# Performance work log

Measured on AMD Instinct MI355X. Metric: run time of the kernel, lower is better.

The kernel has to match this reference:

```python
import jax, jax.numpy as jnp
import numpy as np

B, H_, W_, C, HEADS, WS, SR = 4, 56, 56, 256, 8, 3, 4
HD = C // HEADS
N = H_ * W_
LL = WS * WS
PH, PW = H_ // SR, W_ // SR
PL = PH * PW
K_TAB = 2048


def _unfold3(x, H, W):
    # x: (B, C, H, W) -> (B, C, 9, H*W); matches torch nn.Unfold(kernel_size=3, padding=1)
    xp = jnp.pad(x, ((0, 0), (0, 0), (1, 1), (1, 1)))
    pats = jnp.stack([xp[:, :, i:i + H, j:j + W] for i in range(3) for j in range(3)], axis=2)
    return pats.reshape(x.shape[0], x.shape[1], 9, H * W)


def _l2n(x):
    # torch F.normalize(dim=-1) with eps=1e-12
    return x / jnp.maximum(jnp.linalg.norm(x, axis=-1, keepdims=True), 1e-12)


def setup_inputs() -> dict:
    key = jax.random.key(0)
    ks = jax.random.split(key, 24)
    x = jax.random.normal(ks[0], (B, N, C), jnp.float32)
    # padding mask from unfold of ones image (True where window element falls outside)
    ones = np.zeros((H_ + 2, W_ + 2), np.float32)
    ones[1:-1, 1:-1] = 1.0
    pats = np.stack([ones[i:i + H_, j:j + W_] for i in range(3) for j in range(3)], 0).reshape(9, N)
    padding_mask = jnp.asarray((pats == 0).T)  # (N, 9) bool
    local_valid = LL - padding_mask.sum(-1)
    seq_length_scale = jnp.log(local_valid.astype(jnp.float32) + PL)[:, None]  # (N,1)
    relative_pos_index = jax.random.randint(ks[1], (N * PL,), 0, K_TAB)
    relative_coords_table = jax.random.uniform(ks[2], (K_TAB, 2), jnp.float32, -1.0, 1.0)
    w = lambda k, shape: jax.random.normal(k, shape, jnp.float32) * 0.02
    inp = dict(
        x=x, H=H_, W=W_,
        relative_pos_index=relative_pos_index,
        relative_coords_table=relative_coords_table,
        seq_length_scale=seq_length_scale,
        padding_mask=padding_mask,
        q_w=w(ks[3], (C, C)), q_b=jnp.zeros((C,), jnp.float32),
        kv_w=w(ks[4], (2 * C, C)), kv_b=jnp.zeros((2 * C,), jnp.float32),
        sr_w=w(ks[5], (C, C)), sr_b=jnp.zeros((C,), jnp.float32),
        norm_g=jnp.ones((C,), jnp.float32), norm_b=jnp.zeros((C,), jnp.float32),
        cpb1_w=w(ks[6], (512, 2)), cpb1_b=jnp.zeros((512,), jnp.float32),
        cpb2_w=w(ks[7], (HEADS, 512)), cpb2_b=jnp.zeros((HEADS,), jnp.float32),
        temperature=jnp.log(jnp.exp(jnp.ones((HEADS, 1, 1), jnp.float32) / 0.24) - 1.0),
        query_embedding=w(ks[8], (HEADS, 1, HD)),
        rel_pos_bias_local=jax.random.normal(ks[9], (HEADS, LL), jnp.float32) * 0.0004,
        learnable_tokens=w(ks[10], (HEADS, HD, LL)),
        learnable_bias=jnp.zeros((HEADS, 1, LL), jnp.float32),
        proj_w=w(ks[11], (C, C)), proj_b=jnp.zeros((C,), jnp.float32),
    )
    return inp


def reference(x, H, W, relative_pos_index, relative_coords_table, seq_length_scale,
              padding_mask, q_w, q_b, kv_w, kv_b, sr_w, sr_b, norm_g, norm_b,
              cpb1_w, cpb1_b, cpb2_w, cpb2_b, temperature, query_embedding,
              rel_pos_bias_local, learnable_tokens, learnable_bias, proj_w, proj_b):
    Bsz, n, Cd = x.shape
    h, hd, ll = HEADS, HD, LL
    pH, pW = H // SR, W // SR
    pL = pH * pW
    # ----- queries -----
    q = (x @ q_w.T + q_b).reshape(Bsz, n, h, hd).transpose(0, 2, 1, 3)  # (B,h,N,d)
    q_norm = _l2n(q)
    q_scaled = (q_norm + query_embedding) * jax.nn.softplus(temperature) * seq_length_scale
    # ----- local branch: unfolded window KV -----
    kv = x @ kv_w.T + kv_b  # (B,N,2C)
    k_loc, v_loc = jnp.split(kv, 2, axis=-1)
    k_loc = _l2n(k_loc.reshape(Bsz, n, h, hd)).reshape(Bsz, n, Cd)
    kv_img = jnp.concatenate([k_loc, v_loc], -1).transpose(0, 2, 1).reshape(Bsz, 2 * Cd, H, W)
    pats = _unfold3(kv_img, H, W).reshape(Bsz, 2 * h, hd, ll, n).transpose(0, 1, 4, 2, 3)  # (B,2h,N,d,ll)
    k_local, v_local = jnp.split(pats, 2, axis=1)
    attn_local = jnp.einsum('bhnd,bhndl->bhnl', q_scaled, k_local) + rel_pos_bias_local[:, None, :]
    attn_local = jnp.where(padding_mask, -jnp.inf, attn_local)
    # ----- global branch: 1x1 conv -> GELU -> avg pool -> LN -> KV -----
    x_img = x.transpose(0, 2, 1).reshape(Bsz, Cd, H, W)
    x_sr = jax.nn.gelu(jnp.einsum('oc,bchw->bohw', sr_w, x_img) + sr_b[None, :, None, None], approximate=False)
    x_pool = x_sr.reshape(Bsz, Cd, pH, SR, pW, SR).mean(axis=(3, 5)).reshape(Bsz, Cd, pL).transpose(0, 2, 1)
    mu = x_pool.mean(-1, keepdims=True)
    var = x_pool.var(-1, keepdims=True)
    x_pool = (x_pool - mu) / jnp.sqrt(var + 1e-5) * norm_g + norm_b
    kvp = (x_pool @ kv_w.T + kv_b).reshape(Bsz, pL, 2 * h, hd).transpose(0, 2, 1, 3)
    k_pool, v_pool = jnp.split(kvp, 2, axis=1)  # each (B,h,pL,d)
    # CPB-MLP relative position bias (interpolate is identity since test==trained resolution)
    tab = jax.nn.relu(relative_coords_table @ cpb1_w.T + cpb1_b) @ cpb2_w.T + cpb2_b  # (K,h)
    pool_bias = tab.T[:, relative_pos_index].reshape(h, n, pL)
    attn_pool = jnp.einsum('bhnd,bhmd->bhnm', q_scaled, _l2n(k_pool)) + pool_bias
    # ----- joint softmax over [local | pool] -----
    attn = jax.nn.softmax(jnp.concatenate([attn_local, attn_pool], axis=-1), axis=-1)
    a_loc, a_pool = attn[..., :ll], attn[..., ll:]
    w_loc = jnp.einsum('bhnd,hdl->bhnl', q_norm, learnable_tokens) + learnable_bias + a_loc
    x_local = jnp.einsum('bhnl,bhndl->bhnd', w_loc, v_local)
    x_glob = jnp.einsum('bhnm,bhmd->bhnd', a_pool, v_pool)
    out = (x_local + x_glob).transpose(0, 2, 1, 3).reshape(Bsz, n, Cd)
    return out @ proj_w.T + proj_b
```

## Files before the change

### kernel.cpp

```cpp
#include <hip/hip_runtime.h>
#include <hip/hip_bf16.h>
#include <math.h>

#define Bn   4
#define Hh   56
#define Wn   56
#define Cn   256
#define NHn  8
#define HDn  32
#define Nn   3136
#define LLn  9
#define PLn  196
#define PWn  14
#define KTABn 2048
#define Mrows 12544
#define MP   224

#define XCNT   3211264
#define QWOFF  XCNT
#define KVWOFF (QWOFF + 65536)
#define SRWOFF (KVWOFF + 131072)
#define PWOFF  (SRWOFF + 65536)
#define TOTCVT (PWOFF + 65536)

typedef __attribute__((ext_vector_type(8))) short short8v;
typedef __attribute__((ext_vector_type(4))) float float4v;

__device__ __forceinline__ unsigned short f2b(float f) {
  __hip_bfloat16 h = __float2bfloat16(f);
  return *(unsigned short*)&h;
}
__device__ __forceinline__ float b2f(unsigned short u) {
  union { unsigned int i; float f; } x; x.i = ((unsigned int)u) << 16; return x.f;
}
__device__ __forceinline__ void u4_to8f(uint4 u, float* o) {
  o[0]=b2f((unsigned short)(u.x&0xffff)); o[1]=b2f((unsigned short)(u.x>>16));
  o[2]=b2f((unsigned short)(u.y&0xffff)); o[3]=b2f((unsigned short)(u.y>>16));
  o[4]=b2f((unsigned short)(u.z&0xffff)); o[5]=b2f((unsigned short)(u.z>>16));
  o[6]=b2f((unsigned short)(u.w&0xffff)); o[7]=b2f((unsigned short)(u.w>>16));
}

__launch_bounds__(256)
__global__ void cvt5(const float* __restrict__ x, const float* __restrict__ qw,
                     const float* __restrict__ kvw, const float* __restrict__ srw,
                     const float* __restrict__ pw, unsigned short* __restrict__ dst)
{
  const int i = (blockIdx.x * 256 + threadIdx.x) * 4;
  const float* src; int off;
  if      (i < XCNT)   { src = x;   off = 0; }
  else if (i < KVWOFF) { src = qw;  off = QWOFF; }
  else if (i < SRWOFF) { src = kvw; off = KVWOFF; }
  else if (i < PWOFF)  { src = srw; off = SRWOFF; }
  else                 { src = pw;  off = PWOFF; }
  const float4 v = *(const float4*)(src + (i - off));
  ushort4 o2;
  o2.x = f2b(v.x); o2.y = f2b(v.y); o2.z = f2b(v.z); o2.w = f2b(v.w);
  *(ushort4*)(dst + i) = o2;
}

template <int MODE>
__launch_bounds__(512)
__global__ void mgemm(const unsigned short* __restrict__ A,
                      const unsigned short* __restrict__ Wb,
                      const float* __restrict__ b0, const float* __restrict__ b1,
                      const float* __restrict__ b2, void* __restrict__ Cv, int Nc,
                      const float* __restrict__ sls, const float* __restrict__ qe,
                      const float* __restrict__ temp, float* __restrict__ Mq)
{
  __shared__ __align__(16) unsigned char smem[34816];
  unsigned short* As = (unsigned short*)smem;
  unsigned short* Bs = (unsigned short*)(smem + 16384);
  const int t = threadIdx.x;
  const int w = t >> 6, lane = t & 63;
  const int q = lane >> 4, ln = lane & 15;
  const int n0 = blockIdx.x * 128, m0 = blockIdx.y * 128;
  const int wm = (w >> 1) * 32, wn = (w & 1) * 64;

  float4v acc[2][4];
  #pragma unroll
  for (int mt = 0; mt < 2; ++mt)
    #pragma unroll
    for (int nt = 0; nt < 4; ++nt)
      acc[mt][nt] = (float4v){0.f, 0.f, 0.f, 0.f};

  for (int k0 = 0; k0 < 256; k0 += 64) {
    #pragma unroll
    for (int j = 0; j < 2; ++j) {
      const int u = t + 512 * j;
      const int r = u >> 3, cg = u & 7;
      const int cs = cg ^ (r & 7);
      const uint4 av = *(const uint4*)(A  + (size_t)(m0 + r) * 256 + k0 + cg * 8);
      *(uint4*)(As + r * 64 + cs * 8) = av;
      const uint4 bv = *(const uint4*)(Wb + (size_t)(n0 + r) * 256 + k0 + cg * 8);
      *(uint4*)(Bs + r * 64 + cs * 8) = bv;
    }
    __syncthreads();
    #pragma unroll
    for (int kk = 0; kk < 2; ++kk) {
      short8v af[2], bfr[4];
      const int cg = kk * 4 + q;
      #pragma unroll
      for (int mt = 0; mt < 2; ++mt) {
        const int r = wm + mt * 16 + ln;
        af[mt] = *(const short8v*)(As + r * 64 + (cg ^ (r & 7)) * 8);
      }
      #pragma unroll
      for (int nt = 0; nt < 4; ++nt) {
        const int r = wn + nt * 16 + ln;
        bfr[nt] = *(const short8v*)(Bs + r * 64 + (cg ^ (r & 7)) * 8);
      }
      #pragma unroll
      for (int mt = 0; mt < 2; ++mt)
        #pragma unroll
        for (int nt = 0; nt < 4; ++nt)
          acc[mt][nt] = __builtin_amdgcn_mfma_f32_16x16x32_bf16(af[mt], bfr[nt], acc[mt][nt], 0, 0, 0);
    }
    __syncthreads();
  }

  if constexpr (MODE == 0) {
    float* C = (float*)Cv;
    float* tileF = (float*)smem;
    float bia[4];
    #pragma unroll
    for (int nt = 0; nt < 4; ++nt) bia[nt] = b0[n0 + wn + nt * 16 + ln];
    #pragma unroll
    for (int half = 0; half < 2; ++half) {
      if ((w >> 2) == half) {
        #pragma unroll
        for (int mt = 0; mt < 2; ++mt)
          #pragma unroll
          for (int r = 0; r < 4; ++r)
            #pragma unroll
            for (int nt = 0; nt < 4; ++nt)
              tileF[(wm - half*64 + mt*16 + q*4 + r) * 132 + wn + nt*16 + ln] = acc[mt][nt][r] + bia[nt];
      }
      __syncthreads();
      #pragma unroll
      for (int j = 0; j < 4; ++j) {
        const int i = j * 512 + t;
        const int row = i >> 5, ch = i & 31;
        float4 v = *(const float4*)(tileF + row * 132 + ch * 4);
        *(float4*)(C + (size_t)(m0 + half * 64 + row) * Nc + n0 + ch * 4) = v;
      }
      __syncthreads();
    }
  } else {
    unsigned short* Cb = (unsigned short*)Cv;
    unsigned short* tileC = (unsigned short*)smem;
    const int seg = n0 >> 8;
    const int h0 = (n0 + wn) >> 5, h1 = h0 + 1;
    float spt0 = 0.f, spt1 = 0.f;
    if (seg == 0) { spt0 = log1pf(__expf(temp[h0])); spt1 = log1pf(__expf(temp[h1])); }
    float bia[4], qev[4];
    #pragma unroll
    for (int nt = 0; nt < 4; ++nt) {
      const int col = n0 + wn + nt * 16 + ln;
      bia[nt] = (seg == 0) ? b0[col] : (seg == 3 ? b2[col - 768] : b1[col - 256]);
      if (seg == 0) qev[nt] = qe[col];
    }
    #pragma unroll
    for (int mt = 0; mt < 2; ++mt) {
      #pragma unroll
      for (int r = 0; r < 4; ++r) {
        const int row = m0 + wm + mt * 16 + q * 4 + r;
        const int lrow = wm + mt * 16 + q * 4 + r;
        float vals[4];
        #pragma unroll
        for (int nt = 0; nt < 4; ++nt) vals[nt] = acc[mt][nt][r] + bia[nt];
        if (seg == 0) {
          float ss0 = vals[0]*vals[0] + vals[1]*vals[1];
          float ss1 = vals[2]*vals[2] + vals[3]*vals[3];
          #pragma unroll
          for (int mk = 1; mk <= 8; mk <<= 1) { ss0 += __shfl_xor(ss0, mk); ss1 += __shfl_xor(ss1, mk); }
          const float i0 = 1.f / fmaxf(sqrtf(ss0), 1e-12f);
          const float i1 = 1.f / fmaxf(sqrtf(ss1), 1e-12f);
          const int nidx = row % Nn, bb = row / Nn;
          const float sl = sls[nidx];
          float qsv[4];
          #pragma unroll
          for (int nt = 0; nt < 4; ++nt) {
            const float inv = (nt < 2) ? i0 : i1;
            const float sp  = (nt < 2) ? spt0 : spt1;
            qsv[nt] = (vals[nt] * inv + qev[nt]) * sp * sl;
          }
          float t0 = qsv[0]*qsv[0] + qsv[1]*qsv[1];
          float t1 = qsv[2]*qsv[2] + qsv[3]*qsv[3];
          #pragma unroll
          for (int mk = 1; mk <= 8; mk <<= 1) { t0 += __shfl_xor(t0, mk); t1 += __shfl_xor(t1, mk); }
          if (ln == 0) {
            Mq[((size_t)(bb * NHn + h0)) * Nn + nidx] = sqrtf(t0);
            Mq[((size_t)(bb * NHn + h1)) * Nn + nidx] = sqrtf(t1);
          }
          #pragma unroll
          for (int nt = 0; nt < 4; ++nt)
            tileC[lrow * 136 + wn + nt*16 + ln] = f2b(qsv[nt]);
        } else if (seg == 1) {
          float ss0 = vals[0]*vals[0] + vals[1]*vals[1];
          float ss1 = vals[2]*vals[2] + vals[3]*vals[3];
          #pragma unroll
          for (int mk = 1; mk <= 8; mk <<= 1) { ss0 += __shfl_xor(ss0, mk); ss1 += __shfl_xor(ss1, mk); }
          const float i0 = 1.f / fmaxf(sqrtf(ss0), 1e-12f);
          const float i1 = 1.f / fmaxf(sqrtf(ss1), 1e-12f);
          #pragma unroll
          for (int nt = 0; nt < 4; ++nt)
            tileC[lrow * 136 + wn + nt*16 + ln] = f2b(vals[nt] * ((nt < 2) ? i0 : i1));
        } else if (seg == 2) {
          #pragma unroll
          for (int nt = 0; nt < 4; ++nt)
            tileC[lrow * 136 + wn + nt*16 + ln] = f2b(vals[nt]);
        } else {
          #pragma unroll
          for (int nt = 0; nt < 4; ++nt) {
            const float v = vals[nt];
            tileC[lrow * 136 + wn + nt*16 + ln] =
              f2b(0.5f * v * (1.0f + erff(v * 0.70710678118654752f)));
          }
        }
      }
    }
    __syncthreads();
    #pragma unroll
    for (int j = 0; j < 4; ++j) {
      const int i = j * 512 + t;
      const int row = i >> 4, ch = i & 15;
      uint4 v = *(const uint4*)(tileC + row * 136 + ch * 8);
      *(uint4*)(Cb + (size_t)(m0 + row) * 1024 + n0 + ch * 8) = v;
    }
  }
}

__launch_bounds__(256)
__global__ void gemm_k(const float* __restrict__ A, const float* __restrict__ W,
                       const float* __restrict__ bias, float* __restrict__ Co,
                       int Mr, int Nc, int K)
{
  __shared__ __align__(16) float As[16][64];
  __shared__ __align__(16) float Ws[16][64];
  const int t  = threadIdx.x;
  const int m0 = blockIdx.y * 64, n0 = blockIdx.x * 64;
  const int lm = t >> 2, lk = (t & 3) << 2;
  const int tx = t & 15, ty = t >> 4;
  float acc[4][4] = {};
  int arow = m0 + lm; if (arow >= Mr) arow = Mr - 1;
  const int wrow = n0 + lm;
  for (int k0 = 0; k0 < K; k0 += 16) {
    float4 av = *(const float4*)(A + (size_t)arow * K + k0 + lk);
    As[lk+0][lm] = av.x; As[lk+1][lm] = av.y; As[lk+2][lm] = av.z; As[lk+3][lm] = av.w;
    float4 wv = *(const float4*)(W + (size_t)wrow * K + k0 + lk);
    Ws[lk+0][lm] = wv.x; Ws[lk+1][lm] = wv.y; Ws[lk+2][lm] = wv.z; Ws[lk+3][lm] = wv.w;
    __syncthreads();
    #pragma unroll
    for (int k = 0; k < 16; ++k) {
      float4 a = *(const float4*)&As[k][ty << 2];
      float4 w = *(const float4*)&Ws[k][tx << 2];
      acc[0][0] += a.x*w.x; acc[0][1] += a.x*w.y; acc[0][2] += a.x*w.z; acc[0][3] += a.x*w.w;
      acc[1][0] += a.y*w.x; acc[1][1] += a.y*w.y; acc[1][2] += a.y*w.z; acc[1][3] += a.y*w.w;
      acc[2][0] += a.z*w.x; acc[2][1] += a.z*w.y; acc[2][2] += a.z*w.z; acc[2][3] += a.z*w.w;
      acc[3][0] += a.w*w.x; acc[3][1] += a.w*w.y; acc[3][2] += a.w*w.z; acc[3][3] += a.w*w.w;
    }
    __syncthreads();
  }
  #pragma unroll
  for (int i = 0; i < 4; ++i) {
    const int row = m0 + (ty << 2) + i;
    if (row >= Mr) continue;
    #pragma unroll
    for (int j = 0; j < 4; ++j) {
      const int col = n0 + (tx << 2) + j;
      Co[(size_t)row * Nc + col] = acc[i][j] + bias[col];
    }
  }
}

__launch_bounds__(256)
__global__ void pool_ln_k(const unsigned short* __restrict__ fused, float* __restrict__ pln,
                          const float* __restrict__ g, const float* __restrict__ bb)
{
  const int blk = blockIdx.x;
  const int b = blk / PLn, pc = blk % PLn;
  const int pi = pc / PWn, pj = pc % PWn;
  const int c = threadIdx.x;
  float s = 0.f;
  #pragma unroll
  for (int r = 0; r < 4; ++r)
    #pragma unroll
    for (int cc = 0; cc < 4; ++cc) {
      const int n = (pi*4 + r) * Wn + pj*4 + cc;
      s += b2f(fused[((size_t)b * Nn + n) * 1024 + 768 + c]);
    }
  s *= (1.f/16.f);
  float sum = s, sq = s*s;
  #pragma unroll
  for (int m = 32; m >= 1; m >>= 1) { sum += __shfl_xor(sum, m); sq += __shfl_xor(sq, m); }
  __shared__ float sm[8];
  const int lane = c & 63, wid = c >> 6;
  if (lane == 0) { sm[wid] = sum; sm[4+wid] = sq; }
  __syncthreads();
  const float tot  = sm[0]+sm[1]+sm[2]+sm[3];
  const float totq = sm[4]+sm[5]+sm[6]+sm[7];
  const float mu  = tot * (1.f/256.f);
  const float var = totq * (1.f/256.f) - mu*mu;
  pln[(size_t)blk * Cn + c] = (s - mu) / sqrtf(var + 1e-5f) * g[c] + bb[c];
}

__launch_bounds__(256)
__global__ void pool_pack(const float* __restrict__ kvp, unsigned short* __restrict__ kbf,
                          unsigned short* __restrict__ vbf)
{
  const int bh = blockIdx.x;
  const int b = bh >> 3, h = bh & 7;
  const int t = threadIdx.x, mg = t >> 5, d = t & 31;
  for (int mi = 0; mi < MP/8; ++mi) {
    const int m = mi * 8 + mg;
    float kv2 = 0.f, vv = 0.f;
    if (m < PLn) {
      kv2 = kvp[((size_t)(b * PLn + m)) * 512 + h * HDn + d];
      vv  = kvp[((size_t)(b * PLn + m)) * 512 + 256 + h * HDn + d];
    }
    float ssn = kv2 * kv2;
    #pragma unroll
    for (int mm = 16; mm >= 1; mm >>= 1) ssn += __shfl_xor(ssn, mm);
    const float kn = (m < PLn) ? kv2 / fmaxf(sqrtf(ssn), 1e-12f) : 0.f;
    kbf[((size_t)bh * MP + m) * HDn + d] = f2b(kn);
    vbf[((size_t)bh * 33 + d) * MP + m] = f2b(vv);
  }
  for (int i = t; i < MP; i += 256)
    vbf[((size_t)bh * 33 + 32) * MP + i] = f2b(1.0f);
}

__launch_bounds__(64)
__global__ void cpb_k(const float* __restrict__ rct, const float* __restrict__ w1,
                      const float* __restrict__ b1, const float* __restrict__ w2,
                      const float* __restrict__ b2, float* __restrict__ tab)
{
  const int r = blockIdx.x, t = threadIdx.x;
  const float c0 = rct[r*2], c1 = rct[r*2+1];
  float part[8] = {};
  #pragma unroll
  for (int jj = 0; jj < 8; ++jj) {
    const int j = t * 8 + jj;
    float hv = fmaxf(c0 * w1[j*2] + c1 * w1[j*2+1] + b1[j], 0.f);
    #pragma unroll
    for (int h = 0; h < 8; ++h) part[h] += hv * w2[h*512 + j];
  }
  #pragma unroll
  for (int h = 0; h < 8; ++h)
    for (int mm = 32; mm >= 1; mm >>= 1) part[h] += __shfl_xor(part[h], mm);
  if (t < 8) tab[r*8 + t] = part[t] + b2[t];
}

__launch_bounds__(256)
__global__ void redmax_k(const float* __restrict__ tab, const float* __restrict__ rpb,
                         float* __restrict__ scal)
{
  float mx = -1e30f;
  for (int i = threadIdx.x; i < KTABn*NHn; i += 256) mx = fmaxf(mx, tab[i]);
  if (threadIdx.x < NHn*LLn) mx = fmaxf(mx, rpb[threadIdx.x]);
  #pragma unroll
  for (int m = 32; m >= 1; m >>= 1) mx = fmaxf(mx, __shfl_xor(mx, m));
  __shared__ float sm[4];
  if ((threadIdx.x & 63) == 0) sm[threadIdx.x >> 6] = mx;
  __syncthreads();
  if (threadIdx.x == 0) scal[0] = fmaxf(fmaxf(sm[0], sm[1]), fmaxf(sm[2], sm[3]));
}

__launch_bounds__(256)
__global__ void bias_g2(const int* __restrict__ rpi, const float* __restrict__ tab,
                        unsigned short* __restrict__ bias2)
{
  const int tid = blockIdx.x * 256 + threadIdx.x;
  const int n = tid / MP, m = tid - n * MP;
  if (m < PLn) {
    const int idx = rpi[(size_t)n * PLn + m];
    #pragma unroll
    for (int h = 0; h < NHn; ++h)
      bias2[((size_t)h * Nn + n) * MP + m] = f2b(tab[(size_t)idx * NHn + h]);
  } else {
    #pragma unroll
    for (int h = 0; h < NHn; ++h)
      bias2[((size_t)h * Nn + n) * MP + m] = 0xFF80;
  }
}

__launch_bounds__(256)
__global__ void attn_f(const unsigned short* __restrict__ fused,
                       const unsigned short* __restrict__ kbf,
                       const unsigned short* __restrict__ vbf,
                       const unsigned short* __restrict__ bias2,
                       const float* __restrict__ Mq, const float* __restrict__ scal,
                       const float* __restrict__ slsp, const float* __restrict__ temp,
                       const float* __restrict__ qe, const float* __restrict__ lt,
                       const float* __restrict__ lb, const float* __restrict__ rpb,
                       unsigned short* __restrict__ outp)
{
  __shared__ __align__(16) unsigned short sh[32256];
  unsigned short* k_lds = sh;
  unsigned short* v_lds = sh + 7168;
  unsigned short* p_lds = sh + 17920;
  float* tabf = (float*)(v_lds + 33 * MP);
  float* qe_s  = tabf;
  float* lt_s  = tabf + 32;
  float* lb_s  = tabf + 320;
  float* rpb_s = tabf + 329;
  const int t = threadIdx.x;
  const int w = t >> 6, lane = t & 63;
  const int ln = lane & 15, quad = lane >> 4;
  const int tile = blockIdx.x, h = blockIdx.y, b = blockIdx.z;
  const int bh = b * NHn + h;

  {
    const uint4* gk = (const uint4*)(kbf + (size_t)bh * (MP * HDn));
    uint4* lk = (uint4*)k_lds;
    for (int i = t; i < 896; i += 256) lk[i] = gk[i];
    const uint4* gv = (const uint4*)(vbf + (size_t)bh * (33 * MP));
    uint4* lv = (uint4*)v_lds;
    for (int i = t; i < 924; i += 256) lv[i] = gv[i];
    if (t < 32) qe_s[t] = qe[h * HDn + t];
    for (int i = t; i < HDn * LLn; i += 256) lt_s[i] = lt[h * HDn * LLn + i];
    if (t < LLn) { lb_s[t] = lb[h * LLn + t]; rpb_s[t] = rpb[h * LLn + t]; }
  }
  __syncthreads();

  const int nb = tile * 64 + w * 16;
  const short8v afrag = *(const short8v*)(fused +
      ((size_t)(b * Nn + nb + ln)) * 1024 + h * HDn + quad * 8);
  float M4[4];
  const float sc = scal[0];
  #pragma unroll
  for (int r = 0; r < 4; ++r) M4[r] = Mq[(size_t)bh * Nn + nb + quad * 4 + r] + sc;

  unsigned short* pst = p_lds + w * (16 * MP);
  #pragma unroll
  for (int mt = 0; mt < 14; ++mt) {
    short8v bfrag = *(const short8v*)(k_lds + (mt * 16 + ln) * HDn + quad * 8);
    float4v s = __builtin_amdgcn_mfma_f32_16x16x32_bf16(afrag, bfrag,
                                                        (float4v){0.f,0.f,0.f,0.f}, 0, 0, 0);
    #pragma unroll
    for (int r = 0; r < 4; ++r) {
      const int nr = nb + quad * 4 + r;
      const float bv = b2f(bias2[((size_t)h * Nn + nr) * MP + mt * 16 + ln]);
      const float p = __expf(s[r] + bv - M4[r]);
      pst[(quad * 4 + r) * MP + mt * 16 + ln] = f2b(p);
    }
  }

  float4v accO[3];
  accO[0] = (float4v){0.f,0.f,0.f,0.f};
  accO[1] = (float4v){0.f,0.f,0.f,0.f};
  accO[2] = (float4v){0.f,0.f,0.f,0.f};
  #pragma unroll
  for (int kc = 0; kc < 7; ++kc) {
    short8v pa = *(const short8v*)(pst + ln * MP + kc * 32 + quad * 8);
    #pragma unroll
    for (int nt = 0; nt < 3; ++nt) {
      short8v vb = *(const short8v*)(v_lds + (nt * 16 + ln) * MP + kc * 32 + quad * 8);
      accO[nt] = __builtin_amdgcn_mfma_f32_16x16x32_bf16(pa, vb, accO[nt], 0, 0, 0);
    }
  }
  float* pool_w = (float*)pst;
  #pragma unroll
  for (int r = 0; r < 4; ++r) {
    const int row = quad * 4 + r;
    pool_w[row * 33 + ln]      = accO[0][r];
    pool_w[row * 33 + 16 + ln] = accO[1][r];
    if (ln == 0) pool_w[row * 33 + 32] = accO[2][r];
  }

  const int nl = t >> 2, dg = t & 3;
  const int n = tile * 64 + nl;
  const unsigned short* qp = fused + ((size_t)(b * Nn + n)) * 1024 + h * HDn + dg * 8;
  float qs8[8];
  u4_to8f(*(const uint4*)qp, qs8);
  const float M = Mq[(size_t)bh * Nn + n] + sc;
  const float spt = log1pf(__expf(temp[h]));
  const float inv_qs = 1.f / (spt * slsp[n]);

  float acc8[8], ext8[8];
  #pragma unroll
  for (int j = 0; j < 8; ++j) { acc8[j] = 0.f; ext8[j] = 0.f; }
  float l_run = 0.f;
  const int pi = n / Wn, pj = n % Wn;
  #pragma unroll
  for (int lc = 0; lc < LLn; ++lc) {
    const int ii = pi + lc/3 - 1, jj = pj + (lc%3) - 1;
    if (ii < 0 || ii >= Hh || jj < 0 || jj >= Wn) continue;
    const int nb2 = ii * Wn + jj;
    const unsigned short* kr = fused + ((size_t)(b * Nn + nb2)) * 1024 + 256 + h * HDn + dg * 8;
    float kk8[8], vv8[8];
    u4_to8f(*(const uint4*)kr, kk8);
    u4_to8f(*(const uint4*)(kr + 256), vv8);
    float pp = 0.f, ep = 0.f;
    #pragma unroll
    for (int j = 0; j < 8; ++j) {
      pp += qs8[j] * kk8[j];
      ep += (qs8[j] * inv_qs - qe_s[dg*8 + j]) * lt_s[(dg*8 + j) * LLn + lc];
    }
    pp += __shfl_xor(pp, 1); pp += __shfl_xor(pp, 2);
    ep += __shfl_xor(ep, 1); ep += __shfl_xor(ep, 2);
    const float e = ep + lb_s[lc];
    const float p = __expf(pp + rpb_s[lc] - M);
    l_run += p;
    #pragma unroll
    for (int j = 0; j < 8; ++j) { acc8[j] += p * vv8[j]; ext8[j] += e * vv8[j]; }
  }

  const float* pool_r = (float*)(p_lds + w * (16 * MP)) + (nl - w * 16) * 33;
  const float l_pool = pool_r[32];
  const float invl = 1.f / (l_run + l_pool);
  uint4 u;
  {
    const float* op = pool_r + dg * 8;
    float o0 = (acc8[0]+op[0])*invl + ext8[0], o1 = (acc8[1]+op[1])*invl + ext8[1];
    float o2 = (acc8[2]+op[2])*invl + ext8[2], o3 = (acc8[3]+op[3])*invl + ext8[3];
    float o4 = (acc8[4]+op[4])*invl + ext8[4], o5 = (acc8[5]+op[5])*invl + ext8[5];
    float o6 = (acc8[6]+op[6])*invl + ext8[6], o7 = (acc8[7]+op[7])*invl + ext8[7];
    u.x = f2b(o0) | ((unsigned int)f2b(o1) << 16);
    u.y = f2b(o2) | ((unsigned int)f2b(o3) << 16);
    u.z = f2b(o4) | ((unsigned int)f2b(o5) << 16);
    u.w = f2b(o6) | ((unsigned int)f2b(o7) << 16);
  }
  *(uint4*)(outp + ((size_t)b * Nn + n) * Cn + h * HDn + dg * 8) = u;
}

extern "C" void kernel_launch(void* const* d_in, const int* in_sizes, int n_in,
                              void* d_out, int out_size, void* d_ws, size_t ws_size,
                              hipStream_t stream)
{
  const float* x    = (const float*)d_in[0];
  const int*   rpi  = (const int*)d_in[3];
  const float* rct  = (const float*)d_in[4];
  const float* sls  = (const float*)d_in[5];
  const float* q_w  = (const float*)d_in[7];
  const float* q_b  = (const float*)d_in[8];
  const float* kv_w = (const float*)d_in[9];
  const float* kv_b = (const float*)d_in[10];
  const float* sr_w = (const float*)d_in[11];
  const float* sr_b = (const float*)d_in[12];
  const float* ng   = (const float*)d_in[13];
  const float* nbta = (const float*)d_in[14];
  const float* c1w  = (const float*)d_in[15];
  const float* c1b  = (const float*)d_in[16];
  const float* c2w  = (const float*)d_in[17];
  const float* c2b  = (const float*)d_in[18];
  const float* temp = (const float*)d_in[19];
  const float* qe   = (const float*)d_in[20];
  const float* rpb  = (const float*)d_in[21];
  const float* lt   = (const float*)d_in[22];
  const float* lb   = (const float*)d_in[23];
  const float* pw   = (const float*)d_in[24];
  const float* pb   = (const float*)d_in[25];

  float* ws = (float*)d_ws;
  size_t o = 0;
  unsigned short* bf = (unsigned short*)(ws + o); o += TOTCVT / 2;
  unsigned short* fused = (unsigned short*)(ws + o); o += (size_t)Mrows * 512;
  float* Mq    = ws + o;  o += (size_t)Bn * NHn * Nn;
  float* pln   = ws + o;  o += (size_t)Bn * PLn * Cn;
  float* kvp   = ws + o;  o += (size_t)Bn * PLn * 2 * Cn;
  unsigned short* kbf = (unsigned short*)(ws + o); o += (size_t)Bn * NHn * MP * HDn / 2;
  unsigned short* vbf = (unsigned short*)(ws + o); o += (size_t)Bn * NHn * 33 * MP / 2;
  float* tab   = ws + o;  o += (size_t)KTABn * NHn;
  float* scal  = ws + o;  o += 8;
  unsigned short* bias2 = (unsigned short*)(ws + o); o += (size_t)NHn * Nn * MP / 2;
  unsigned short* outp  = (unsigned short*)(ws + o); o += (size_t)Mrows * Cn / 2;

  const unsigned short* xbf   = bf;
  const unsigned short* qkvsw = bf + QWOFF;
  const unsigned short* pwbf  = bf + PWOFF;

  cvt5<<<TOTCVT/1024, 256, 0, stream>>>(x, q_w, kv_w, sr_w, pw, bf);
  mgemm<1><<<dim3(8, 98), 512, 0, stream>>>(xbf, qkvsw, q_b, kv_b, sr_b, fused, 1024,
                                            sls, qe, temp, Mq);
  pool_ln_k<<<Bn*PLn, 256, 0, stream>>>(fused, pln, ng, nbta);
  gemm_k<<<dim3(8, 13), 256, 0, stream>>>(pln, kv_w, kv_b, kvp, Bn*PLn, 512, 256);
  pool_pack<<<Bn*NHn, 256, 0, stream>>>(kvp, kbf, vbf);
  cpb_k<<<KTABn, 64, 0, stream>>>(rct, c1w, c1b, c2w, c2b, tab);
  redmax_k<<<1, 256, 0, stream>>>(tab, rpb, scal);
  bias_g2<<<(Nn*MP)/256, 256, 0, stream>>>(rpi, tab, bias2);
  attn_f<<<dim3(49, NHn, Bn), 256, 0, stream>>>(fused, kbf, vbf, bias2, Mq, scal,
                                                sls, temp, qe, lt, lb, rpb, outp);
  mgemm<0><<<dim3(2, 98), 512, 0, stream>>>(outp, pwbf, pb, pb, pb, (float*)d_out, 256,
                                            nullptr, nullptr, nullptr, nullptr);
}
```

Measured before the change: 261.5 us.

## Retile mgemm to 256 threads with register prefetch and fuse table max into cpb

The bf16 MFMA GEMM now runs 256 threads per block. Each wave computes a 64x64 sub-tile (4x4 MFMA tiles) instead of 32x64, so more fragments are reused from shared memory. The next K slice is prefetched from global memory into registers while the current slice is computed, overlapping load latency with MFMA work. The separate single-block redmax kernel is removed: cpb_k computes the bias-table maximum with a wave reduction and an integer atomicMax on a zero-initialised scalar. That max now ignores the local relative-position bias and is clamped at zero, which changes the stabiliser value, and the larger per-wave tile raises register pressure.

```diff
diff --git a/kernel.cpp b/kernel.cpp
--- a/kernel.cpp
+++ b/kernel.cpp
@@ -59,7 +59,7 @@
 }
 
 template <int MODE>
-__launch_bounds__(512)
+__launch_bounds__(256)
 __global__ void mgemm(const unsigned short* __restrict__ A,
                       const unsigned short* __restrict__ Wb,
                       const float* __restrict__ b0, const float* __restrict__ b1,
@@ -74,33 +74,49 @@
   const int w = t >> 6, lane = t & 63;
   const int q = lane >> 4, ln = lane & 15;
   const int n0 = blockIdx.x * 128, m0 = blockIdx.y * 128;
-  const int wm = (w >> 1) * 32, wn = (w & 1) * 64;
-
-  float4v acc[2][4];
-  #pragma unroll
-  for (int mt = 0; mt < 2; ++mt)
+  const int wm = (w >> 1) * 64, wn = (w & 1) * 64;
+
+  float4v acc[4][4];
+  #pragma unroll
+  for (int mt = 0; mt < 4; ++mt)
     #pragma unroll
     for (int nt = 0; nt < 4; ++nt)
       acc[mt][nt] = (float4v){0.f, 0.f, 0.f, 0.f};
 
+  int srow[4], scg[4];
+  #pragma unroll
+  for (int j = 0; j < 4; ++j) {
+    const int u = t + 256 * j;
+    srow[j] = u >> 3; scg[j] = u & 7;
+  }
+  uint4 avr[4], bvr[4];
+  #pragma unroll
+  for (int j = 0; j < 4; ++j) {
+    avr[j] = *(const uint4*)(A  + (size_t)(m0 + srow[j]) * 256 + scg[j] * 8);
+    bvr[j] = *(const uint4*)(Wb + (size_t)(n0 + srow[j]) * 256 + scg[j] * 8);
+  }
+
   for (int k0 = 0; k0 < 256; k0 += 64) {
     #pragma unroll
-    for (int j = 0; j < 2; ++j) {
-      const int u = t + 512 * j;
-      const int r = u >> 3, cg = u & 7;
-      const int cs = cg ^ (r & 7);
-      const uint4 av = *(const uint4*)(A  + (size_t)(m0 + r) * 256 + k0 + cg * 8);
-      *(uint4*)(As + r * 64 + cs * 8) = av;
-      const uint4 bv = *(const uint4*)(Wb + (size_t)(n0 + r) * 256 + k0 + cg * 8);
-      *(uint4*)(Bs + r * 64 + cs * 8) = bv;
+    for (int j = 0; j < 4; ++j) {
+      const int cs = scg[j] ^ (srow[j] & 7);
+      *(uint4*)(As + srow[j] * 64 + cs * 8) = avr[j];
+      *(uint4*)(Bs + srow[j] * 64 + cs * 8) = bvr[j];
     }
     __syncthreads();
+    if (k0 < 192) {
+      #pragma unroll
+      for (int j = 0; j < 4; ++j) {
+        avr[j] = *(const uint4*)(A  + (size_t)(m0 + srow[j]) * 256 + k0 + 64 + scg[j] * 8);
+        bvr[j] = *(const uint4*)(Wb + (size_t)(n0 + srow[j]) * 256 + k0 + 64 + scg[j] * 8);
+      }
+    }
     #pragma unroll
     for (int kk = 0; kk < 2; ++kk) {
-      short8v af[2], bfr[4];
+      short8v af[4], bfr[4];
       const int cg = kk * 4 + q;
       #pragma unroll
-      for (int mt = 0; mt < 2; ++mt) {
+      for (int mt = 0; mt < 4; ++mt) {
         const int r = wm + mt * 16 + ln;
         af[mt] = *(const short8v*)(As + r * 64 + (cg ^ (r & 7)) * 8);
       }
@@ -110,7 +126,7 @@
         bfr[nt] = *(const short8v*)(Bs + r * 64 + (cg ^ (r & 7)) * 8);
       }
       #pragma unroll
-      for (int mt = 0; mt < 2; ++mt)
+      for (int mt = 0; mt < 4; ++mt)
         #pragma unroll
         for (int nt = 0; nt < 4; ++nt)
           acc[mt][nt] = __builtin_amdgcn_mfma_f32_16x16x32_bf16(af[mt], bfr[nt], acc[mt][nt], 0, 0, 0);
@@ -126,19 +142,19 @@
     for (int nt = 0; nt < 4; ++nt) bia[nt] = b0[n0 + wn + nt * 16 + ln];
     #pragma unroll
     for (int half = 0; half < 2; ++half) {
-      if ((w >> 2) == half) {
+      if ((w >> 1) == half) {
         #pragma unroll
-        for (int mt = 0; mt < 2; ++mt)
+        for (int mt = 0; mt < 4; ++mt)
           #pragma unroll
           for (int r = 0; r < 4; ++r)
             #pragma unroll
             for (int nt = 0; nt < 4; ++nt)
-              tileF[(wm - half*64 + mt*16 + q*4 + r) * 132 + wn + nt*16 + ln] = acc[mt][nt][r] + bia[nt];
+              tileF[(mt*16 + q*4 + r) * 132 + wn + nt*16 + ln] = acc[mt][nt][r] + bia[nt];
       }
       __syncthreads();
       #pragma unroll
-      for (int j = 0; j < 4; ++j) {
-        const int i = j * 512 + t;
+      for (int j = 0; j < 8; ++j) {
+        const int i = j * 256 + t;
         const int row = i >> 5, ch = i & 31;
         float4 v = *(const float4*)(tileF + row * 132 + ch * 4);
         *(float4*)(C + (size_t)(m0 + half * 64 + row) * Nc + n0 + ch * 4) = v;
@@ -160,7 +176,7 @@
       if (seg == 0) qev[nt] = qe[col];
     }
     #pragma unroll
-    for (int mt = 0; mt < 2; ++mt) {
+    for (int mt = 0; mt < 4; ++mt) {
       #pragma unroll
       for (int r = 0; r < 4; ++r) {
         const int row = m0 + wm + mt * 16 + q * 4 + r;
@@ -221,8 +237,8 @@
     }
     __syncthreads();
     #pragma unroll
-    for (int j = 0; j < 4; ++j) {
-      const int i = j * 512 + t;
+    for (int j = 0; j < 8; ++j) {
+      const int i = j * 256 + t;
       const int row = i >> 4, ch = i & 15;
       uint4 v = *(const uint4*)(tileC + row * 136 + ch * 8);
       *(uint4*)(Cb + (size_t)(m0 + row) * 1024 + n0 + ch * 8) = v;
@@ -332,7 +348,8 @@
 __launch_bounds__(64)
 __global__ void cpb_k(const float* __restrict__ rct, const float* __restrict__ w1,
                       const float* __restrict__ b1, const float* __restrict__ w2,
-                      const float* __restrict__ b2, float* __restrict__ tab)
+                      const float* __restrict__ b2, float* __restrict__ tab,
+                      float* __restrict__ scal)
 {
   const int r = blockIdx.x, t = threadIdx.x;
   const float c0 = rct[r*2], c1 = rct[r*2+1];
@@ -347,22 +364,11 @@
   #pragma unroll
   for (int h = 0; h < 8; ++h)
     for (int mm = 32; mm >= 1; mm >>= 1) part[h] += __shfl_xor(part[h], mm);
-  if (t < 8) tab[r*8 + t] = part[t] + b2[t];
-}
-
-__launch_bounds__(256)
-__global__ void redmax_k(const float* __restrict__ tab, const float* __restrict__ rpb,
-                         float* __restrict__ scal)
-{
-  float mx = -1e30f;
-  for (int i = threadIdx.x; i < KTABn*NHn; i += 256) mx = fmaxf(mx, tab[i]);
-  if (threadIdx.x < NHn*LLn) mx = fmaxf(mx, rpb[threadIdx.x]);
-  #pragma unroll
-  for (int m = 32; m >= 1; m >>= 1) mx = fmaxf(mx, __shfl_xor(mx, m));
-  __shared__ float sm[4];
-  if ((threadIdx.x & 63) == 0) sm[threadIdx.x >> 6] = mx;
-  __syncthreads();
-  if (threadIdx.x == 0) scal[0] = fmaxf(fmaxf(sm[0], sm[1]), fmaxf(sm[2], sm[3]));
+  float v = -1e30f;
+  if (t < 8) { const float o = part[t] + b2[t]; tab[r*8 + t] = o; v = o; }
+  #pragma unroll
+  for (int mm = 32; mm >= 1; mm >>= 1) v = fmaxf(v, __shfl_xor(v, mm));
+  if (t == 0 && v > 0.f) atomicMax((int*)scal, __float_as_int(v));
 }
 
 __launch_bounds__(256)
@@ -569,17 +575,17 @@
   const unsigned short* qkvsw = bf + QWOFF;
   const unsigned short* pwbf  = bf + PWOFF;
 
+  hipMemsetAsync(scal, 0, sizeof(float), stream);
   cvt5<<<TOTCVT/1024, 256, 0, stream>>>(x, q_w, kv_w, sr_w, pw, bf);
-  mgemm<1><<<dim3(8, 98), 512, 0, stream>>>(xbf, qkvsw, q_b, kv_b, sr_b, fused, 1024,
+  mgemm<1><<<dim3(8, 98), 256, 0, stream>>>(xbf, qkvsw, q_b, kv_b, sr_b, fused, 1024,
                                             sls, qe, temp, Mq);
   pool_ln_k<<<Bn*PLn, 256, 0, stream>>>(fused, pln, ng, nbta);
   gemm_k<<<dim3(8, 13), 256, 0, stream>>>(pln, kv_w, kv_b, kvp, Bn*PLn, 512, 256);
   pool_pack<<<Bn*NHn, 256, 0, stream>>>(kvp, kbf, vbf);
-  cpb_k<<<KTABn, 64, 0, stream>>>(rct, c1w, c1b, c2w, c2b, tab);
-  redmax_k<<<1, 256, 0, stream>>>(tab, rpb, scal);
+  cpb_k<<<KTABn, 64, 0, stream>>>(rct, c1w, c1b, c2w, c2b, tab, scal);
   bias_g2<<<(Nn*MP)/256, 256, 0, stream>>>(rpi, tab, bias2);
   attn_f<<<dim3(49, NHn, Bn), 256, 0, stream>>>(fused, kbf, vbf, bias2, Mq, scal,
                                                 sls, temp, qe, lt, lb, rpb, outp);
-  mgemm<0><<<dim3(2, 98), 512, 0, stream>>>(outp, pwbf, pb, pb, pb, (float*)d_out, 256,
+  mgemm<0><<<dim3(2, 98), 256, 0, stream>>>(outp, pwbf, pb, pb, pb, (float*)d_out, 256,
                                             nullptr, nullptr, nullptr, nullptr);
 }
```

Result: slower. 314.2 us (+20.2%).
